# Kernel optimization log

Hardware: AMD Instinct MI355X
Metric: run time of the kernel (lower is better)

Reference implementation:

```python
import jax, jax.numpy as jnp
import numpy as np

OUT, IN = 4096, 4096          # weight_shape
T, K, GROUP = 256, 2, 256     # trellis window, bits/weight, weight_scales_group_size
GRID = np.array([-3.0, -1.0, 1.0, 3.0], dtype=np.float32) / np.sqrt(5.0)  # 2-bit symmetric, unit-power


def fwht(x):
    """Normalized fast Walsh-Hadamard transform along the last axis (H = H^T, orthonormal)."""
    n = x.shape[-1]
    orig = x.shape
    y = x.reshape(-1, n)
    rows = y.shape[0]
    h = 1
    while h < n:
        y = y.reshape(rows, n // (2 * h), 2, h)
        a, b = y[:, :, 0, :], y[:, :, 1, :]
        y = jnp.stack([a + b, a - b], axis=2)
        h *= 2
    return y.reshape(orig) * (1.0 / np.sqrt(n)).astype(np.float32)


def fake_quant_u8_per_channel(x):
    """InputQuantizer: 8-bit PER_CHANNEL asymmetric fake-quant over the last (in-channel) dim."""
    red = tuple(range(x.ndim - 1))
    xmin = jnp.min(x, axis=red)
    xmax = jnp.max(x, axis=red)
    scale = jnp.maximum((xmax - xmin) / 255.0, 1e-8)
    zero = jnp.round(-xmin / scale)
    q = jnp.clip(jnp.round(x / scale) + zero, 0.0, 255.0)
    dq = (q - zero) * scale
    # straight-through estimator (matches torch fake-quant training behavior)
    return x + jax.lax.stop_gradient(dq - x)


def decode_trellis(trellis):
    """LowBitSym decode: unpack K=2-bit codes from packed 16-bit trellis words and map
    to the symmetric unit-power 2-bit grid. trellis: (NV, T//16*K) int -> (OUT, IN) float."""
    shifts = jnp.arange(14, -1, -2, dtype=jnp.int32)         # MSB-first 2-bit fields
    codes = (trellis[:, :, None] >> shifts) & 3               # (NV, 32, 8)
    grid = jnp.asarray(GRID)
    return grid[codes].reshape(OUT, IN)


def setup_inputs() -> dict:
    key = jax.random.key(0)
    k1, k2, k3, k4, k5 = jax.random.split(key, 5)
    x = jax.random.normal(k1, (4, 2048, IN), dtype=jnp.float32)
    SU = jax.random.normal(k2, (IN,), dtype=jnp.float32)
    SV = jax.random.normal(k3, (OUT,), dtype=jnp.float32)
    weight_scales = jax.random.uniform(k4, (OUT * IN // GROUP, 1), dtype=jnp.float32)
    trellis = jax.random.randint(k5, (OUT * IN // T, T // 16 * K), 0, 65536, dtype=jnp.int32)
    return {"x": x, "SU": SU, "SV": SV, "weight_scales": weight_scales, "trellis": trellis}


def reference(x, SU, SV, weight_scales, trellis):
    # activation path: incoherence rotate + 8-bit fake quant
    xh = fwht(x * SU)                       # matmul_hadUt_cuda(x * SU)
    xq = fake_quant_u8_per_channel(xh)
    # weight path: trellis decode + Hadamard + SV + grouped scales
    w = decode_trellis(trellis)             # (OUT, IN)
    w = (fwht(w.T) * SV).T                  # (matmul_hadU_cuda(w.T) * SV).T
    w = (w.reshape(-1, GROUP) * weight_scales).reshape(OUT, IN)
    # F.linear(input=xq, weight=w)
    return jnp.einsum('bsi,oi->bso', xq, w)
```

## Files before the change

### kernel.cpp

```cpp
#include <hip/hip_runtime.h>
#include <hip/hip_bf16.h>
#include <stdint.h>

#define IN_DIM 4096
#define OUT_DIM 4096
#define M_ROWS 8192

typedef __attribute__((ext_vector_type(8))) short s16x8;
typedef __attribute__((ext_vector_type(4))) float f32x4;

__device__ __forceinline__ unsigned short f2bf(float f) {
  uint32_t u = __float_as_uint(f);
  uint32_t r = (u + 0x7fffu + ((u >> 16) & 1u)) >> 16;
  return (unsigned short)r;
}

__device__ __forceinline__ void async16(void* lds, const void* g) {
  __builtin_amdgcn_global_load_lds(
      (const __attribute__((address_space(1))) unsigned int*)g,
      (__attribute__((address_space(3))) unsigned int*)lds, 16, 0, 0);
}

#define FENCE asm volatile("" ::: "memory")

__device__ __forceinline__ void h16(float (&v)[16]) {
#pragma unroll
  for (int h = 1; h < 16; h <<= 1) {
#pragma unroll
    for (int g = 0; g < 8; ++g) {
      int r = g & (h - 1);
      int i0 = ((g & ~(h - 1)) << 1) | r;
      float a = v[i0], b = v[i0 + h];
      v[i0] = a + b;
      v[i0 + h] = a - b;
    }
  }
}

__global__ void fwht_x_kernel(const float* __restrict__ x, const float* __restrict__ SU,
                              float* __restrict__ xh) {
  __shared__ float s[4352];
  const int row = blockIdx.x;
  const int t = threadIdx.x;
  float v[16];
  const float4* xr  = (const float4*)(x + (size_t)row * IN_DIM);
  const float4* su4 = (const float4*)SU;
#pragma unroll
  for (int q = 0; q < 4; ++q) {
    float4 a = xr[t * 4 + q], sv = su4[t * 4 + q];
    v[q * 4 + 0] = a.x * sv.x;
    v[q * 4 + 1] = a.y * sv.y;
    v[q * 4 + 2] = a.z * sv.z;
    v[q * 4 + 3] = a.w * sv.w;
  }
  h16(v);
#pragma unroll
  for (int c = 0; c < 16; ++c) {
    int i = t * 16 + c;
    s[i + (i >> 4)] = v[c];
  }
  __syncthreads();
  const int A = t >> 4, C = t & 15;
#pragma unroll
  for (int b = 0; b < 16; ++b) {
    int i = A * 256 + b * 16 + C;
    v[b] = s[i + (i >> 4)];
  }
  h16(v);
  __syncthreads();
#pragma unroll
  for (int b = 0; b < 16; ++b) {
    int i = A * 256 + b * 16 + C;
    s[i + (i >> 4)] = v[b];
  }
  __syncthreads();
#pragma unroll
  for (int a = 0; a < 16; ++a) {
    int i = a * 256 + t;
    v[a] = s[i + (i >> 4)];
  }
  h16(v);
  float* orow = xh + (size_t)row * IN_DIM;
#pragma unroll
  for (int a = 0; a < 16; ++a) orow[a * 256 + t] = v[a] * 0.015625f;
}

__global__ void minmax_part_kernel(const float* __restrict__ xh,
                                   float* __restrict__ pmin, float* __restrict__ pmax) {
  const int rc = blockIdx.x >> 4;
  const int cb = blockIdx.x & 15;
  const int ch = cb * 256 + threadIdx.x;
  float mn = 3.4e38f, mx = -3.4e38f;
  const float* base = xh + (size_t)rc * 256 * IN_DIM + ch;
  for (int r = 0; r < 256; ++r) {
    float v = base[(size_t)r * IN_DIM];
    mn = fminf(mn, v);
    mx = fmaxf(mx, v);
  }
  pmin[rc * IN_DIM + ch] = mn;
  pmax[rc * IN_DIM + ch] = mx;
}

__global__ void minmax_fin_kernel(const float* __restrict__ pmin, const float* __restrict__ pmax,
                                  float* __restrict__ scale, float* __restrict__ zero) {
  int ch = blockIdx.x * 256 + threadIdx.x;
  float mn = 3.4e38f, mx = -3.4e38f;
  for (int rc = 0; rc < 32; ++rc) {
    mn = fminf(mn, pmin[rc * IN_DIM + ch]);
    mx = fmaxf(mx, pmax[rc * IN_DIM + ch]);
  }
  float sc = fmaxf((mx - mn) / 255.0f, 1e-8f);
  float zp = rintf(-mn / sc);
  scale[ch] = sc;
  zero[ch] = zp;
}

__global__ void quant_kernel(const float* __restrict__ xh, const float* __restrict__ scale,
                             const float* __restrict__ zero, unsigned short* __restrict__ xq) {
  const int total4 = M_ROWS * IN_DIM / 4;
  for (int i4 = blockIdx.x * blockDim.x + threadIdx.x; i4 < total4;
       i4 += gridDim.x * blockDim.x) {
    int c4 = i4 & (IN_DIM / 4 - 1);
    float4 v  = ((const float4*)xh)[i4];
    float4 sc = ((const float4*)scale)[c4];
    float4 zp = ((const float4*)zero)[c4];
    float q0 = fminf(fmaxf(rintf(v.x / sc.x) + zp.x, 0.f), 255.f);
    float q1 = fminf(fmaxf(rintf(v.y / sc.y) + zp.y, 0.f), 255.f);
    float q2 = fminf(fmaxf(rintf(v.z / sc.z) + zp.z, 0.f), 255.f);
    float q3 = fminf(fmaxf(rintf(v.w / sc.w) + zp.w, 0.f), 255.f);
    ushort4 o;
    o.x = f2bf((q0 - zp.x) * sc.x);
    o.y = f2bf((q1 - zp.y) * sc.y);
    o.z = f2bf((q2 - zp.z) * sc.z);
    o.w = f2bf((q3 - zp.w) * sc.w);
    ((ushort4*)xq)[i4] = o;
  }
}

#define W_RADIX4(TARR)                                                     \
  for (int h = 1; h < 64; h <<= 2) {                                       \
    __syncthreads();                                                       \
    _Pragma("unroll") for (int j = 0; j < 4; ++j) {                        \
      int g = j * 256 + tid;                                               \
      int c = g & 63, u = g >> 6;                                          \
      int r = u & (h - 1);                                                 \
      int i0 = ((u & ~(h - 1)) << 2) | r;                                  \
      float a = TARR[i0][c], b2 = TARR[i0 + h][c];                         \
      float c2 = TARR[i0 + 2 * h][c], d = TARR[i0 + 3 * h][c];             \
      float y0 = a + b2, y1 = a - b2, y2 = c2 + d, y3 = c2 - d;            \
      TARR[i0][c] = y0 + y2;                                               \
      TARR[i0 + h][c] = y1 + y3;                                           \
      TARR[i0 + 2 * h][c] = y0 - y2;                                       \
      TARR[i0 + 3 * h][c] = y1 - y3;                                       \
    }                                                                      \
  }                                                                        \
  __syncthreads();

__global__ void fwht_w_inner_fused(const int* __restrict__ trellis, float* __restrict__ w) {
  __shared__ float t[64][65];
  const int ohi = blockIdx.x >> 6;
  const int it  = blockIdx.x & 63;
  const int tid = threadIdx.x;
  const float g = 0.44721359549995793f;
#pragma unroll
  for (int j = 0; j < 2; ++j) {
    int wi = j * 256 + tid;
    int r = wi >> 3, wc = wi & 7;
    int word = trellis[(size_t)(ohi * 64 + r) * 512 + it * 8 + wc];
#pragma unroll
    for (int jj = 0; jj < 8; ++jj) {
      int code = (word >> (14 - 2 * jj)) & 3;
      t[r][wc * 8 + jj] = (float)(2 * code - 3) * g;
    }
  }
  W_RADIX4(t)
#pragma unroll
  for (int j = 0; j < 16; ++j) {
    int e = j * 256 + tid;
    int r = e >> 6, c = e & 63;
    w[((size_t)(ohi * 64 + r)) * IN_DIM + it * 64 + c] = t[r][c];
  }
}

__global__ void fwht_w_outer(const float* __restrict__ w, const float* __restrict__ SV,
                             const float* __restrict__ wscale, unsigned short* __restrict__ wq) {
  __shared__ float t[64][65];
  const int olo = blockIdx.x >> 6;
  const int it  = blockIdx.x & 63;
  const int tid = threadIdx.x;
#pragma unroll
  for (int j = 0; j < 16; ++j) {
    int e = j * 256 + tid;
    int r = e >> 6, c = e & 63;
    t[r][c] = w[((size_t)(r * 64 + olo)) * IN_DIM + it * 64 + c];
  }
  W_RADIX4(t)
#pragma unroll
  for (int j = 0; j < 16; ++j) {
    int e = j * 256 + tid;
    int r = e >> 6, c = e & 63;
    int o = r * 64 + olo;
    int i = it * 64 + c;
    float val = t[r][c] * 0.015625f * SV[o] * wscale[(o << 4) + (i >> 8)];
    wq[(size_t)o * IN_DIM + i] = f2bf(val);
  }
}

__global__ __launch_bounds__(512, 2) void gemm256_kernel(
    const unsigned short* __restrict__ A, const unsigned short* __restrict__ B,
    float* __restrict__ C) {
  __shared__ __align__(16) unsigned short lds[65536];
  const int tid  = threadIdx.x;
  const int lane = tid & 63;
  const int wave = tid >> 6;
  const int wm = wave >> 2, wn = wave & 3;
  const int fr = lane & 15, kqi = lane >> 4;
  const int swz = fr & 7;

  const int b  = blockIdx.x;
  const int wg = (b & 7) * 64 + (b >> 3);
  const int bm = wg >> 4, bn = wg & 15;
  const int gm0 = bm * 256, gn0 = bn * 256;

  f32x4 acc[2][2][4][2] = {};
  s16x8 af[4][2];
  s16x8 bf[2][2][2];

  const int F0 = tid, F1 = 512 + tid;
  const int rh0 = F0 >> 3, s0 = (F0 & 7) ^ (rh0 & 7);
  const int rh1 = F1 >> 3, s1 = (F1 & 7) ^ (rh1 & 7);
  auto stage = [&](const unsigned short* gbase, int grow0, int kcol, int ldsoff) {
    async16((void*)&lds[ldsoff + F0 * 8],
            (const void*)(gbase + (size_t)(grow0 + rh0) * IN_DIM + kcol + s0 * 8));
    async16((void*)&lds[ldsoff + F1 * 8],
            (const void*)(gbase + (size_t)(grow0 + rh1) * IN_DIM + kcol + s1 * 8));
  };

#define READ_AF(QM, TBUF)                                                                \
  {                                                                                      \
    const int abase = (TBUF) * 16384 + (QM) * 8192;                                      \
    _Pragma("unroll") for (int kk = 0; kk < 2; ++kk)                                     \
      _Pragma("unroll") for (int mi = 0; mi < 4; ++mi) {                                 \
        int rh = wm * 64 + mi * 16 + fr;                                                 \
        af[mi][kk] = *(const s16x8*)&lds[abase + rh * 64 + (((kk * 4 + kqi) ^ swz) * 8)];\
      }                                                                                  \
  }
#define READ_BF(QN, TBUF)                                                                \
  {                                                                                      \
    const int bbase = 32768 + (TBUF) * 16384 + (QN) * 8192;                              \
    _Pragma("unroll") for (int kk = 0; kk < 2; ++kk)                                     \
      _Pragma("unroll") for (int ni = 0; ni < 2; ++ni) {                                 \
        int rh = wn * 32 + ni * 16 + fr;                                                 \
        bf[QN][ni][kk] =                                                                 \
            *(const s16x8*)&lds[bbase + rh * 64 + (((kk * 4 + kqi) ^ swz) * 8)];         \
      }                                                                                  \
  }
#define ENDPHASE(QM, QN, SGBASE, SGROW0, SKCOL, SLDSOFF, VM)                             \
  {                                                                                      \
    stage(SGBASE, SGROW0, SKCOL, SLDSOFF);                                               \
    FENCE;                                                                               \
    asm volatile("s_waitcnt vmcnt(" #VM ")" ::: "memory");                               \
    __builtin_amdgcn_s_barrier();                                                        \
    FENCE;                                                                               \
    __builtin_amdgcn_s_setprio(1);                                                       \
    _Pragma("unroll") for (int kk = 0; kk < 2; ++kk)                                     \
      _Pragma("unroll") for (int mi = 0; mi < 4; ++mi)                                   \
        _Pragma("unroll") for (int ni = 0; ni < 2; ++ni)                                 \
          acc[QM][QN][mi][ni] = __builtin_amdgcn_mfma_f32_16x16x32_bf16(                 \
              af[mi][kk], bf[QN][ni][kk], acc[QM][QN][mi][ni], 0, 0, 0);                 \
    __builtin_amdgcn_s_setprio(0);                                                       \
    FENCE;                                                                               \
    __builtin_amdgcn_s_barrier();                                                        \
    FENCE;                                                                               \
  }

  stage(A, gm0,       0, 0);
  stage(B, gn0,       0, 32768);
  stage(A, gm0 + 128, 0, 8192);
  stage(B, gn0 + 128, 0, 40960);
  stage(A, gm0,      64, 16384);
  stage(B, gn0,      64, 49152);
  FENCE;
  asm volatile("s_waitcnt vmcnt(8)" ::: "memory");
  __builtin_amdgcn_s_barrier();
  FENCE;

  for (int it = 0; it < 32; ++it) {
    const int k1 = ((2 * it + 1) * 64) & 4095;
    const int k2 = ((2 * it + 2) * 64) & 4095;
    const int k3 = ((2 * it + 3) * 64) & 4095;
    READ_AF(0, 0) READ_BF(0, 0)
    ENDPHASE(0, 0, A, gm0 + 128, k1, 24576, 6)
    READ_BF(1, 0)
    ENDPHASE(0, 1, B, gn0 + 128, k1, 57344, 63)
    READ_AF(1, 0)
    ENDPHASE(1, 1, A, gm0,       k2, 0,     63)
    ENDPHASE(1, 0, B, gn0,       k2, 32768, 8)
    READ_AF(0, 1) READ_BF(0, 1)
    ENDPHASE(0, 0, A, gm0 + 128, k2, 8192,  6)
    READ_BF(1, 1)
    ENDPHASE(0, 1, B, gn0 + 128, k2, 40960, 63)
    READ_AF(1, 1)
    ENDPHASE(1, 1, A, gm0,       k3, 16384, 63)
    ENDPHASE(1, 0, B, gn0,       k3, 49152, 8)
  }
#undef ENDPHASE
#undef READ_AF
#undef READ_BF
  asm volatile("s_waitcnt vmcnt(0)" ::: "memory");

  const int orow = kqi * 4;
#pragma unroll
  for (int qm = 0; qm < 2; ++qm)
#pragma unroll
    for (int qn = 0; qn < 2; ++qn)
#pragma unroll
      for (int mi = 0; mi < 4; ++mi)
#pragma unroll
        for (int ni = 0; ni < 2; ++ni) {
          const int row0 = gm0 + qm * 128 + wm * 64 + mi * 16 + orow;
          const int col  = gn0 + qn * 128 + wn * 32 + ni * 16 + fr;
          f32x4 v = acc[qm][qn][mi][ni];
#pragma unroll
          for (int r = 0; r < 4; ++r)
            C[(size_t)(row0 + r) * OUT_DIM + col] = v[r];
        }
}

extern "C" void kernel_launch(void* const* d_in, const int* in_sizes, int n_in,
                              void* d_out, int out_size, void* d_ws, size_t ws_size,
                              hipStream_t stream) {
  const float* x      = (const float*)d_in[0];
  const float* SU     = (const float*)d_in[1];
  const float* SV     = (const float*)d_in[2];
  const float* wscale = (const float*)d_in[3];
  const int* trellis  = (const int*)d_in[4];
  float* out = (float*)d_out;

  char* ws = (char*)d_ws;
  unsigned short* xq = (unsigned short*)ws;
  unsigned short* wq = (unsigned short*)(ws + (size_t)67108864);
  float* pmin  = (float*)(ws + (size_t)67108864);
  float* pmax  = (float*)(ws + (size_t)67108864 + 524288);
  float* scale = (float*)(ws + (size_t)67108864 + 1048576);
  float* zero  = (float*)(ws + (size_t)67108864 + 1064960);

  float* xh   = out;
  float* wdec = out;

  hipLaunchKernelGGL(fwht_x_kernel, dim3(M_ROWS), dim3(256), 0, stream, x, SU, xh);
  hipLaunchKernelGGL(minmax_part_kernel, dim3(512), dim3(256), 0, stream, xh, pmin, pmax);
  hipLaunchKernelGGL(minmax_fin_kernel, dim3(16), dim3(256), 0, stream, pmin, pmax, scale, zero);
  hipLaunchKernelGGL(quant_kernel, dim3(2048), dim3(256), 0, stream, xh, scale, zero, xq);
  hipLaunchKernelGGL(fwht_w_inner_fused, dim3(4096), dim3(256), 0, stream, trellis, wdec);
  hipLaunchKernelGGL(fwht_w_outer, dim3(4096), dim3(256), 0, stream, wdec, SV, wscale, wq);
  hipLaunchKernelGGL(gemm256_kernel, dim3((M_ROWS / 256) * (OUT_DIM / 256)), dim3(512), 0,
                     stream, xq, wq, out);
}
```

Measured before the change: 371.4 us.

## Store intermediates in bf16 and switch GEMM to 32x32x16 MFMA

Stores the Hadamard-rotated activations and the partially transformed weights as bf16 instead of fp32. This halves intermediate memory traffic in the minmax, quant and outer-FWHT kernels, and the x FWHT output order is changed so the stores can be vectorised. The GEMM moves from 16x16x32 to 32x32x16 bf16 MFMA tiles, which changes the fragment layout and the epilogue indexing. Rounding the intermediates to bf16 before the min/max, quantisation and second Hadamard pass adds error and could shift per-channel scales.

After: 383.3 us. 1.03x slower.

```diff
diff --git a/kernel.cpp b/kernel.cpp
--- a/kernel.cpp
+++ b/kernel.cpp
@@ -8,11 +8,15 @@
 
 typedef __attribute__((ext_vector_type(8))) short s16x8;
 typedef __attribute__((ext_vector_type(4))) float f32x4;
+typedef __attribute__((ext_vector_type(16))) float f32x16;
 
 __device__ __forceinline__ unsigned short f2bf(float f) {
   uint32_t u = __float_as_uint(f);
   uint32_t r = (u + 0x7fffu + ((u >> 16) & 1u)) >> 16;
   return (unsigned short)r;
+}
+__device__ __forceinline__ float b2f(unsigned short u) {
+  return __uint_as_float((uint32_t)u << 16);
 }
 
 __device__ __forceinline__ void async16(void* lds, const void* g) {
@@ -38,26 +42,22 @@
 }
 
 __global__ void fwht_x_kernel(const float* __restrict__ x, const float* __restrict__ SU,
-                              float* __restrict__ xh) {
+                              unsigned short* __restrict__ xh) {
   __shared__ float s[4352];
   const int row = blockIdx.x;
   const int t = threadIdx.x;
   float v[16];
-  const float4* xr  = (const float4*)(x + (size_t)row * IN_DIM);
-  const float4* su4 = (const float4*)SU;
-#pragma unroll
-  for (int q = 0; q < 4; ++q) {
-    float4 a = xr[t * 4 + q], sv = su4[t * 4 + q];
-    v[q * 4 + 0] = a.x * sv.x;
-    v[q * 4 + 1] = a.y * sv.y;
-    v[q * 4 + 2] = a.z * sv.z;
-    v[q * 4 + 3] = a.w * sv.w;
+  const float* xr = x + (size_t)row * IN_DIM;
+#pragma unroll
+  for (int a = 0; a < 16; ++a) {
+    int i = a * 256 + t;
+    v[a] = xr[i] * SU[i];
   }
   h16(v);
 #pragma unroll
-  for (int c = 0; c < 16; ++c) {
-    int i = t * 16 + c;
-    s[i + (i >> 4)] = v[c];
+  for (int a = 0; a < 16; ++a) {
+    int i = a * 256 + t;
+    s[i + (i >> 4)] = v[a];
   }
   __syncthreads();
   const int A = t >> 4, C = t & 15;
@@ -75,30 +75,38 @@
   }
   __syncthreads();
 #pragma unroll
-  for (int a = 0; a < 16; ++a) {
-    int i = a * 256 + t;
-    v[a] = s[i + (i >> 4)];
+  for (int c = 0; c < 16; ++c) {
+    int i = t * 16 + c;
+    v[c] = s[i + (i >> 4)];
   }
   h16(v);
-  float* orow = xh + (size_t)row * IN_DIM;
-#pragma unroll
-  for (int a = 0; a < 16; ++a) orow[a * 256 + t] = v[a] * 0.015625f;
-}
-
-__global__ void minmax_part_kernel(const float* __restrict__ xh,
+  unsigned short ob[16];
+#pragma unroll
+  for (int c = 0; c < 16; ++c) ob[c] = f2bf(v[c] * 0.015625f);
+  s16x8* dst = (s16x8*)(xh + (size_t)row * IN_DIM + t * 16);
+  dst[0] = *(s16x8*)&ob[0];
+  dst[1] = *(s16x8*)&ob[8];
+}
+
+__global__ void minmax_part_kernel(const unsigned short* __restrict__ xh,
                                    float* __restrict__ pmin, float* __restrict__ pmax) {
-  const int rc = blockIdx.x >> 4;
-  const int cb = blockIdx.x & 15;
-  const int ch = cb * 256 + threadIdx.x;
-  float mn = 3.4e38f, mx = -3.4e38f;
-  const float* base = xh + (size_t)rc * 256 * IN_DIM + ch;
+  const int rc = blockIdx.x >> 3;
+  const int cb = blockIdx.x & 7;
+  const int ch0 = cb * 512 + threadIdx.x * 2;
+  float mn0 = 3.4e38f, mx0 = -3.4e38f, mn1 = 3.4e38f, mx1 = -3.4e38f;
+  const unsigned int* base =
+      (const unsigned int*)(xh + (size_t)rc * 256 * IN_DIM + ch0);
   for (int r = 0; r < 256; ++r) {
-    float v = base[(size_t)r * IN_DIM];
-    mn = fminf(mn, v);
-    mx = fmaxf(mx, v);
-  }
-  pmin[rc * IN_DIM + ch] = mn;
-  pmax[rc * IN_DIM + ch] = mx;
+    unsigned int u = base[(size_t)r * (IN_DIM / 2)];
+    float v0 = __uint_as_float(u << 16);
+    float v1 = __uint_as_float(u & 0xffff0000u);
+    mn0 = fminf(mn0, v0); mx0 = fmaxf(mx0, v0);
+    mn1 = fminf(mn1, v1); mx1 = fmaxf(mx1, v1);
+  }
+  pmin[rc * IN_DIM + ch0] = mn0;
+  pmin[rc * IN_DIM + ch0 + 1] = mn1;
+  pmax[rc * IN_DIM + ch0] = mx0;
+  pmax[rc * IN_DIM + ch0 + 1] = mx1;
 }
 
 __global__ void minmax_fin_kernel(const float* __restrict__ pmin, const float* __restrict__ pmax,
@@ -115,25 +123,24 @@
   zero[ch] = zp;
 }
 
-__global__ void quant_kernel(const float* __restrict__ xh, const float* __restrict__ scale,
-                             const float* __restrict__ zero, unsigned short* __restrict__ xq) {
-  const int total4 = M_ROWS * IN_DIM / 4;
-  for (int i4 = blockIdx.x * blockDim.x + threadIdx.x; i4 < total4;
-       i4 += gridDim.x * blockDim.x) {
-    int c4 = i4 & (IN_DIM / 4 - 1);
-    float4 v  = ((const float4*)xh)[i4];
-    float4 sc = ((const float4*)scale)[c4];
-    float4 zp = ((const float4*)zero)[c4];
-    float q0 = fminf(fmaxf(rintf(v.x / sc.x) + zp.x, 0.f), 255.f);
-    float q1 = fminf(fmaxf(rintf(v.y / sc.y) + zp.y, 0.f), 255.f);
-    float q2 = fminf(fmaxf(rintf(v.z / sc.z) + zp.z, 0.f), 255.f);
-    float q3 = fminf(fmaxf(rintf(v.w / sc.w) + zp.w, 0.f), 255.f);
-    ushort4 o;
-    o.x = f2bf((q0 - zp.x) * sc.x);
-    o.y = f2bf((q1 - zp.y) * sc.y);
-    o.z = f2bf((q2 - zp.z) * sc.z);
-    o.w = f2bf((q3 - zp.w) * sc.w);
-    ((ushort4*)xq)[i4] = o;
+__global__ void quant_kernel(const unsigned short* __restrict__ xh,
+                             const float* __restrict__ scale, const float* __restrict__ zero,
+                             unsigned short* __restrict__ xq) {
+  const int total8 = M_ROWS * IN_DIM / 8;
+  for (int i8 = blockIdx.x * blockDim.x + threadIdx.x; i8 < total8;
+       i8 += gridDim.x * blockDim.x) {
+    int c8 = i8 & (IN_DIM / 8 - 1);
+    s16x8 v = ((const s16x8*)xh)[i8];
+    unsigned short o[8];
+#pragma unroll
+    for (int j = 0; j < 8; ++j) {
+      float sc = scale[c8 * 8 + j];
+      float zp = zero[c8 * 8 + j];
+      float f = b2f((unsigned short)v[j]);
+      float q = fminf(fmaxf(rintf(f / sc) + zp, 0.f), 255.f);
+      o[j] = f2bf((q - zp) * sc);
+    }
+    ((s16x8*)xq)[i8] = *(s16x8*)&o[0];
   }
 }
 
@@ -156,7 +163,8 @@
   }                                                                        \
   __syncthreads();
 
-__global__ void fwht_w_inner_fused(const int* __restrict__ trellis, float* __restrict__ w) {
+__global__ void fwht_w_inner_fused(const int* __restrict__ trellis,
+                                   unsigned short* __restrict__ w) {
   __shared__ float t[64][65];
   const int ohi = blockIdx.x >> 6;
   const int it  = blockIdx.x & 63;
@@ -178,11 +186,12 @@
   for (int j = 0; j < 16; ++j) {
     int e = j * 256 + tid;
     int r = e >> 6, c = e & 63;
-    w[((size_t)(ohi * 64 + r)) * IN_DIM + it * 64 + c] = t[r][c];
-  }
-}
-
-__global__ void fwht_w_outer(const float* __restrict__ w, const float* __restrict__ SV,
+    w[((size_t)(ohi * 64 + r)) * IN_DIM + it * 64 + c] = f2bf(t[r][c]);
+  }
+}
+
+__global__ void fwht_w_outer(const unsigned short* __restrict__ w,
+                             const float* __restrict__ SV,
                              const float* __restrict__ wscale, unsigned short* __restrict__ wq) {
   __shared__ float t[64][65];
   const int olo = blockIdx.x >> 6;
@@ -192,7 +201,7 @@
   for (int j = 0; j < 16; ++j) {
     int e = j * 256 + tid;
     int r = e >> 6, c = e & 63;
-    t[r][c] = w[((size_t)(r * 64 + olo)) * IN_DIM + it * 64 + c];
+    t[r][c] = b2f(w[((size_t)(r * 64 + olo)) * IN_DIM + it * 64 + c]);
   }
   W_RADIX4(t)
 #pragma unroll
@@ -214,17 +223,21 @@
   const int lane = tid & 63;
   const int wave = tid >> 6;
   const int wm = wave >> 2, wn = wave & 3;
-  const int fr = lane & 15, kqi = lane >> 4;
-  const int swz = fr & 7;
+  const int l31 = lane & 31, lhi = lane >> 5;
+  const int swz = lane & 7;
 
   const int b  = blockIdx.x;
   const int wg = (b & 7) * 64 + (b >> 3);
   const int bm = wg >> 4, bn = wg & 15;
   const int gm0 = bm * 256, gn0 = bn * 256;
 
-  f32x4 acc[2][2][4][2] = {};
-  s16x8 af[4][2];
-  s16x8 bf[2][2][2];
+  f32x16 acc[2][2][2] = {};
+  s16x8 af[2][4];
+  s16x8 bf[2][4];
+
+  const int rha0 = wm * 64 + l31;
+  const int rha1 = wm * 64 + 32 + l31;
+  const int rhb  = wn * 32 + l31;
 
   const int F0 = tid, F1 = 512 + tid;
   const int rh0 = F0 >> 3, s0 = (F0 & 7) ^ (rh0 & 7);
@@ -239,21 +252,16 @@
 #define READ_AF(QM, TBUF)                                                                \
   {                                                                                      \
     const int abase = (TBUF) * 16384 + (QM) * 8192;                                      \
-    _Pragma("unroll") for (int kk = 0; kk < 2; ++kk)                                     \
-      _Pragma("unroll") for (int mi = 0; mi < 4; ++mi) {                                 \
-        int rh = wm * 64 + mi * 16 + fr;                                                 \
-        af[mi][kk] = *(const s16x8*)&lds[abase + rh * 64 + (((kk * 4 + kqi) ^ swz) * 8)];\
-      }                                                                                  \
+    _Pragma("unroll") for (int ks = 0; ks < 4; ++ks) {                                   \
+      af[0][ks] = *(const s16x8*)&lds[abase + rha0 * 64 + (((2 * ks + lhi) ^ swz) * 8)]; \
+      af[1][ks] = *(const s16x8*)&lds[abase + rha1 * 64 + (((2 * ks + lhi) ^ swz) * 8)]; \
+    }                                                                                    \
   }
 #define READ_BF(QN, TBUF)                                                                \
   {                                                                                      \
     const int bbase = 32768 + (TBUF) * 16384 + (QN) * 8192;                              \
-    _Pragma("unroll") for (int kk = 0; kk < 2; ++kk)                                     \
-      _Pragma("unroll") for (int ni = 0; ni < 2; ++ni) {                                 \
-        int rh = wn * 32 + ni * 16 + fr;                                                 \
-        bf[QN][ni][kk] =                                                                 \
-            *(const s16x8*)&lds[bbase + rh * 64 + (((kk * 4 + kqi) ^ swz) * 8)];         \
-      }                                                                                  \
+    _Pragma("unroll") for (int ks = 0; ks < 4; ++ks)                                     \
+      bf[QN][ks] = *(const s16x8*)&lds[bbase + rhb * 64 + (((2 * ks + lhi) ^ swz) * 8)]; \
   }
 #define ENDPHASE(QM, QN, SGBASE, SGROW0, SKCOL, SLDSOFF, VM)                             \
   {                                                                                      \
@@ -263,11 +271,10 @@
     __builtin_amdgcn_s_barrier();                                                        \
     FENCE;                                                                               \
     __builtin_amdgcn_s_setprio(1);                                                       \
-    _Pragma("unroll") for (int kk = 0; kk < 2; ++kk)                                     \
-      _Pragma("unroll") for (int mi = 0; mi < 4; ++mi)                                   \
-        _Pragma("unroll") for (int ni = 0; ni < 2; ++ni)                                 \
-          acc[QM][QN][mi][ni] = __builtin_amdgcn_mfma_f32_16x16x32_bf16(                 \
-              af[mi][kk], bf[QN][ni][kk], acc[QM][QN][mi][ni], 0, 0, 0);                 \
+    _Pragma("unroll") for (int ks = 0; ks < 4; ++ks)                                     \
+      _Pragma("unroll") for (int mt = 0; mt < 2; ++mt)                                   \
+        acc[QM][QN][mt] = __builtin_amdgcn_mfma_f32_32x32x16_bf16(                       \
+            af[mt][ks], bf[QN][ks], acc[QM][QN][mt], 0, 0, 0);                           \
     __builtin_amdgcn_s_setprio(0);                                                       \
     FENCE;                                                                               \
     __builtin_amdgcn_s_barrier();                                                        \
@@ -309,22 +316,21 @@
 #undef READ_BF
   asm volatile("s_waitcnt vmcnt(0)" ::: "memory");
 
-  const int orow = kqi * 4;
 #pragma unroll
   for (int qm = 0; qm < 2; ++qm)
 #pragma unroll
     for (int qn = 0; qn < 2; ++qn)
 #pragma unroll
-      for (int mi = 0; mi < 4; ++mi)
-#pragma unroll
-        for (int ni = 0; ni < 2; ++ni) {
-          const int row0 = gm0 + qm * 128 + wm * 64 + mi * 16 + orow;
-          const int col  = gn0 + qn * 128 + wn * 32 + ni * 16 + fr;
-          f32x4 v = acc[qm][qn][mi][ni];
-#pragma unroll
-          for (int r = 0; r < 4; ++r)
-            C[(size_t)(row0 + r) * OUT_DIM + col] = v[r];
+      for (int mt = 0; mt < 2; ++mt) {
+        f32x16 v = acc[qm][qn][mt];
+        const int col = gn0 + qn * 128 + wn * 32 + l31;
+        const int rbase = gm0 + qm * 128 + wm * 64 + mt * 32 + 4 * lhi;
+#pragma unroll
+        for (int r = 0; r < 16; ++r) {
+          int row = rbase + (r & 3) + 8 * (r >> 2);
+          C[(size_t)row * OUT_DIM + col] = v[r];
         }
+      }
 }
 
 extern "C" void kernel_launch(void* const* d_in, const int* in_sizes, int n_in,
@@ -345,11 +351,11 @@
   float* scale = (float*)(ws + (size_t)67108864 + 1048576);
   float* zero  = (float*)(ws + (size_t)67108864 + 1064960);
 
-  float* xh   = out;
-  float* wdec = out;
+  unsigned short* xh   = (unsigned short*)out;
+  unsigned short* wdec = (unsigned short*)out + (size_t)33554432;
 
   hipLaunchKernelGGL(fwht_x_kernel, dim3(M_ROWS), dim3(256), 0, stream, x, SU, xh);
-  hipLaunchKernelGGL(minmax_part_kernel, dim3(512), dim3(256), 0, stream, xh, pmin, pmax);
+  hipLaunchKernelGGL(minmax_part_kernel, dim3(256), dim3(256), 0, stream, xh, pmin, pmax);
   hipLaunchKernelGGL(minmax_fin_kernel, dim3(16), dim3(256), 0, stream, pmin, pmax, scale, zero);
   hipLaunchKernelGGL(quant_kernel, dim3(2048), dim3(256), 0, stream, xh, scale, zero, xq);
   hipLaunchKernelGGL(fwht_w_inner_fused, dim3(4096), dim3(256), 0, stream, trellis, wdec);
```
